# Optimization experiments

Hardware: AMD Instinct MI355X
Metric: run time of the kernel (lower is better)

The kernel has to match this reference:

```python
import jax, jax.numpy as jnp
import numpy as np

N_CLASSES = 19


def setup_inputs() -> dict:
    key = jax.random.key(0)
    k1, k2 = jax.random.split(key)
    embedding = jax.random.normal(k1, (4, 32, 128, 128), dtype=jnp.float32)
    label = jax.random.randint(k2, (4, 512, 512), 0, N_CLASSES, dtype=jnp.int64)
    return {"embedding": embedding, "label": label}


def _discriminative_loss(embedding, label, n_classes=N_CLASSES):
    N, H, W = label.shape
    C = embedding.shape[1]
    # bilinear upsample embedding to label resolution (F.upsample mode='bilinear')
    emb = jax.image.resize(embedding, (N, C, H, W), method="bilinear")
    HW = H * W
    emb = emb.reshape(N, C, HW).transpose(0, 2, 1)          # (N, HW, C)
    lab = label.reshape(N, HW)                               # (N, HW)

    onehot = jax.nn.one_hot(lab, n_classes, dtype=emb.dtype)  # (N, HW, K)
    count = onehot.sum(1)                                    # (N, K)
    mask = (count > 0).astype(emb.dtype)                     # (N, K)

    # per-class embedding sum and (biased, /(count+1)) mean
    cls_sum = jnp.einsum("npc,npk->nkc", emb, onehot)       # (N, K, C)
    cls_mean = cls_sum / (count[:, :, None] + 1.0)           # (N, K, C)

    # intra-class: per-pixel squared distance to own-class mean, mean over C
    mean_pp = jnp.take_along_axis(cls_mean, lab[:, :, None], axis=1)  # (N, HW, C)
    d2 = jnp.mean((emb - mean_pp) ** 2, axis=-1)             # (N, HW)
    intra_per_cls = jnp.einsum("np,npk->nk", d2, onehot) / (count + 1.0)  # (N, K)
    n_fg = mask[:, 1:].sum(1)                                # (N,)
    l2_intra = (intra_per_cls[:, 1:] * mask[:, 1:]).sum(1) / n_fg  # (N,)

    # inter-class: pairwise mean squared distance between class means
    diff = cls_mean[:, :, None, :] - cls_mean[:, None, :, :]  # (N, K, K, C)
    inter = jnp.mean(diff ** 2, axis=-1)                     # (N, K, K)
    inter = inter * mask[:, None, :] * mask[:, :, None]
    l2_inter = inter[:, 1:, 1:].reshape(N, -1).sum(1) / (n_fg * n_fg)  # (N,)

    return l2_intra - l2_inter


def reference(embedding, label):
    return _discriminative_loss(embedding, label)
```

## Files before the change

### kernel.cpp

```cpp
#include <hip/hip_runtime.h>

#define NIMG 4
#define NCLS 19
#define CCH  32
#define LH   128
#define LW   128
#define HH   512
#define WW   512
#define HWQ  (LH*LW)
#define HWP  (HH*WW)

#define TR 8
#define TC 8
#define NTX (LW/TC)
#define NTILE (256)
#define TCELLS (TR*TC)
#define RW 10
#define RING 100
#define NSLOT 608

__device__ __forceinline__ void taps(int v, int lim, int& i0, float& w0, float& w1) {
    int r = v & 3;
    int b = (v >> 2) + ((r < 2) ? -1 : 0);
    float f = 0.125f + 0.25f * (float)((r + 2) & 3);
    w0 = 1.f - f; w1 = f;
    if (b < 0)           { b = 0;       w0 = 1.f; w1 = 0.f; }
    else if (b >= lim)   { b = lim - 1; w0 = 0.f; w1 = 1.f; }
    i0 = b;
}

__device__ __forceinline__ float ring_fetch(const float* Gn, int i, int Y0, int X0) {
    int p = i / RING, r = i - p * RING;
    int gy = r / RW, gx = r - gy * RW;
    int yy = Y0 - 1 + gy; yy = yy < 0 ? 0 : (yy > LH - 1 ? LH - 1 : yy);
    int xx = X0 - 1 + gx; xx = xx < 0 ? 0 : (xx > LW - 1 ? LW - 1 : xx);
    return Gn[(size_t)p * HWQ + yy * LW + xx];
}

__global__ __launch_bounds__(256) void k_gram(const float* __restrict__ E,
        float* __restrict__ G) {
    int n = blockIdx.y, rp = blockIdx.x;
    int tid = threadIdx.x;
    int x = tid & 127, dy = tid >> 7;
    int y = rp * 2 + dy;
    int yn = (y < LH - 1) ? y + 1 : y;
    int xn = (x < LW - 1) ? x + 1 : x;
    bool fix = ((x & 63) == 63);
    const float* base = E + (size_t)n * CCH * HWQ;
    const float* Ea = base + y * LW + x;
    const float* Eb = base + yn * LW + x;
    const float* Eax = base + y * LW + xn;
    const float* Ebx = base + yn * LW + xn;
    float gs = 0.f, gh = 0.f, gv = 0.f, gda = 0.f;
#pragma unroll 8
    for (int c = 0; c < CCH; c++) {
        float a = Ea[(size_t)c * HWQ];
        float b = Eb[(size_t)c * HWQ];
        float ar = __shfl_down(a, 1);
        float br = __shfl_down(b, 1);
        if (fix) { ar = Eax[(size_t)c * HWQ]; br = Ebx[(size_t)c * HWQ]; }
        gs = fmaf(a, a, gs);
        gh = fmaf(a, ar, gh);
        gv = fmaf(a, b, gv);
        gda = fmaf(a, br, fmaf(ar, b, gda));
    }
    float* Gp = G + (size_t)n * 4 * HWQ + y * LW + x;
    Gp[0] = gs; Gp[HWQ] = gh; Gp[2 * HWQ] = gv; Gp[3 * HWQ] = gda;
}

__global__ __launch_bounds__(256, 4) void k_field(const float* __restrict__ E,
        const int* __restrict__ lab, const float* __restrict__ G,
        float* __restrict__ P_sum, float* __restrict__ P_cnt, float* __restrict__ P_S2) {
    int tile = blockIdx.x, n = blockIdx.y;
    int ty = tile >> 4, tx = tile & 15;
    int Y0 = ty * TR, X0 = tx * TC;
    __shared__ float A[TCELLS * NCLS];
    __shared__ float Gt[4 * RING];
    __shared__ float S2w[4 * NCLS];
    __shared__ float tmpc[NCLS * 8];
    __shared__ __align__(16) float cs_l[NSLOT];
    int tid = threadIdx.x;
    const int* ln = lab + (size_t)n * HWP;
    int h_lo = Y0 * 4 - 2;

    int hA, qA, hB = 0, qB = 0; bool vB;
    int4 LA, LB = make_int4(0, 0, 0, 0);
    {
        int hr = tid / RW, qi = tid - hr * RW;
        hA = h_lo + hr; qA = X0 - 1 + qi;
        int hc = hA < 0 ? 0 : (hA > HH - 1 ? HH - 1 : hA);
        int qc = qA < 0 ? 0 : (qA > LW - 1 ? LW - 1 : qA);
        LA = *(const int4*)(ln + hc * WW + (qc << 2));
    }
    vB = (tid < 360 - 256);
    if (vB) {
        int i = tid + 256;
        int hr = i / RW, qi = i - hr * RW;
        hB = h_lo + hr; qB = X0 - 1 + qi;
        int hc = hB < 0 ? 0 : (hB > HH - 1 ? HH - 1 : hB);
        int qc = qB < 0 ? 0 : (qB > LW - 1 ? LW - 1 : qB);
        LB = *(const int4*)(ln + hc * WW + (qc << 2));
    }
    int cc = tid >> 3, cy = tid & 7;
    const float* Er = E + ((size_t)n * CCH + cc) * HWQ + (Y0 + cy) * LW + X0;
    float4 ev0 = *(const float4*)Er;
    float4 ev1 = *(const float4*)(Er + 4);
    const float* Gn = G + (size_t)n * 4 * HWQ;
    float rv0 = ring_fetch(Gn, tid, Y0, X0);
    bool rB = (tid < 4 * RING - 256);
    float rv1 = rB ? ring_fetch(Gn, tid + 256, Y0, X0) : 0.f;

    for (int i = tid; i < TCELLS * NCLS; i += 256) A[i] = 0.f;
    if (tid < 4 * NCLS) S2w[tid] = 0.f;
    Gt[tid] = rv0;
    if (rB) Gt[tid + 256] = rv1;
    __syncthreads();

    const float* Gs_ = Gt, *Gh_ = Gt + RING, *Gv_ = Gt + 2 * RING, *Gda_ = Gt + 3 * RING;
    auto process = [&](int h, int q, int4 l4) {
        if (h < 0 || h >= HH || q < 0 || q >= LW) return;
        int y0; float wy0, wy1;
        taps(h, LH - 1, y0, wy0, wy1);
        int ry = y0 - Y0;
        bool r0 = (unsigned)ry < (unsigned)TR, r1 = (unsigned)(ry + 1) < (unsigned)TR;
        int rxm = q - 1 - X0, rx0 = q - X0, rxp = q + 1 - X0;
        bool bm = (unsigned)rxm < (unsigned)TC, b0 = (unsigned)rx0 < (unsigned)TC,
             bp = (unsigned)rxp < (unsigned)TC;
        bool fast = (q >= 1) && (q <= 126);
        bool owned = ((unsigned)(h - Y0 * 4) < 32u) && b0;
        if (fast) {
            if (r0) {
                int rb = (ry * TC) * NCLS;
                if (bm) { float* a = &A[rb + rxm * NCLS];
                    atomicAdd(a + l4.x, wy0 * 0.375f); atomicAdd(a + l4.y, wy0 * 0.125f); }
                if (b0) { float* a = &A[rb + rx0 * NCLS];
                    atomicAdd(a + l4.x, wy0 * 0.625f); atomicAdd(a + l4.y, wy0 * 0.875f);
                    atomicAdd(a + l4.z, wy0 * 0.875f); atomicAdd(a + l4.w, wy0 * 0.625f); }
                if (bp) { float* a = &A[rb + rxp * NCLS];
                    atomicAdd(a + l4.z, wy0 * 0.125f); atomicAdd(a + l4.w, wy0 * 0.375f); }
            }
            if (r1) {
                int rb = ((ry + 1) * TC) * NCLS;
                if (bm) { float* a = &A[rb + rxm * NCLS];
                    atomicAdd(a + l4.x, wy1 * 0.375f); atomicAdd(a + l4.y, wy1 * 0.125f); }
                if (b0) { float* a = &A[rb + rx0 * NCLS];
                    atomicAdd(a + l4.x, wy1 * 0.625f); atomicAdd(a + l4.y, wy1 * 0.875f);
                    atomicAdd(a + l4.z, wy1 * 0.875f); atomicAdd(a + l4.w, wy1 * 0.625f); }
                if (bp) { float* a = &A[rb + rxp * NCLS];
                    atomicAdd(a + l4.z, wy1 * 0.125f); atomicAdd(a + l4.w, wy1 * 0.375f); }
            }
            if (owned) {
                float u0 = wy0 * wy0, u1 = wy1 * wy1, u2t = 2.f * wy0 * wy1;
                int g00 = (y0 - Y0 + 1) * RW + rx0;
                float C0 = u0 * Gs_[g00]     + u1 * Gs_[g00 + RW]     + u2t * Gv_[g00];
                float C1 = u0 * Gs_[g00 + 1] + u1 * Gs_[g00 + RW + 1] + u2t * Gv_[g00 + 1];
                float C2 = u0 * Gs_[g00 + 2] + u1 * Gs_[g00 + RW + 2] + u2t * Gv_[g00 + 2];
                float D0 = 2.f * (u0 * Gh_[g00]     + u1 * Gh_[g00 + RW])     + u2t * Gda_[g00];
                float D1 = 2.f * (u0 * Gh_[g00 + 1] + u1 * Gh_[g00 + RW + 1]) + u2t * Gda_[g00 + 1];
                float d2a = fmaf(0.140625f, C0, fmaf(0.390625f, C1, 0.46875f * D0));
                float d2b = fmaf(0.015625f, C0, fmaf(0.765625f, C1, 0.21875f * D0));
                float d2c = fmaf(0.765625f, C1, fmaf(0.015625f, C2, 0.21875f * D1));
                float d2d = fmaf(0.390625f, C1, fmaf(0.140625f, C2, 0.46875f * D1));
                int wv = (tid >> 6) * NCLS;
                atomicAdd(&S2w[wv + l4.x], d2a); atomicAdd(&S2w[wv + l4.y], d2b);
                atomicAdd(&S2w[wv + l4.z], d2c); atomicAdd(&S2w[wv + l4.w], d2d);
            }
        } else {
            int Ls[4] = {l4.x, l4.y, l4.z, l4.w};
            float u0 = wy0 * wy0, u1 = wy1 * wy1, u2t = 2.f * wy0 * wy1;
            int gyr = y0 - Y0 + 1;
            int wv = (tid >> 6) * NCLS;
#pragma unroll
            for (int j = 0; j < 4; j++) {
                int w = (q << 2) + j;
                int x0; float wx0, wx1;
                taps(w, LW - 1, x0, wx0, wx1);
                int rxa = x0 - X0, rxb = rxa + 1;
                int L = Ls[j];
                if (r0) {
                    int rb = (ry * TC) * NCLS;
                    if ((unsigned)rxa < (unsigned)TC) atomicAdd(&A[rb + rxa * NCLS + L], wy0 * wx0);
                    if ((unsigned)rxb < (unsigned)TC) atomicAdd(&A[rb + rxb * NCLS + L], wy0 * wx1);
                }
                if (r1) {
                    int rb = ((ry + 1) * TC) * NCLS;
                    if ((unsigned)rxa < (unsigned)TC) atomicAdd(&A[rb + rxa * NCLS + L], wy1 * wx0);
                    if ((unsigned)rxb < (unsigned)TC) atomicAdd(&A[rb + rxb * NCLS + L], wy1 * wx1);
                }
                if (owned) {
                    int gg = gyr * RW + (x0 - X0 + 1);
                    float Ca = u0 * Gs_[gg]     + u1 * Gs_[gg + RW]     + u2t * Gv_[gg];
                    float Cb = u0 * Gs_[gg + 1] + u1 * Gs_[gg + RW + 1] + u2t * Gv_[gg + 1];
                    float Dd = 2.f * (u0 * Gh_[gg] + u1 * Gh_[gg + RW]) + u2t * Gda_[gg];
                    float d2 = wx0 * wx0 * Ca + wx1 * wx1 * Cb + 2.f * wx0 * wx1 * Dd;
                    atomicAdd(&S2w[wv + L], d2);
                }
            }
        }
    };
    process(hA, qA, LA);
    if (vB) process(hB, qB, LB);
    __syncthreads();

    {
        float ev[8] = {ev0.x, ev0.y, ev0.z, ev0.w, ev1.x, ev1.y, ev1.z, ev1.w};
        float acc[NCLS];
#pragma unroll
        for (int k = 0; k < NCLS; k++) acc[k] = 0.f;
#pragma unroll
        for (int cx = 0; cx < 8; cx++) {
            const float* Ar = &A[(cy * 8 + cx) * NCLS];
            float e = ev[cx];
#pragma unroll
            for (int k = 0; k < NCLS; k++) acc[k] = fmaf(Ar[k], e, acc[k]);
        }
#pragma unroll
        for (int k = 0; k < NCLS; k++) {
            acc[k] += __shfl_xor(acc[k], 1);
            acc[k] += __shfl_xor(acc[k], 2);
            acc[k] += __shfl_xor(acc[k], 4);
        }
        if (cy == 0) {
#pragma unroll
            for (int k = 0; k < NCLS; k++) cs_l[k * CCH + cc] = acc[k];
        }
    }
    if (tid < 8 * NCLS) {
        int g8 = tid / NCLS, k = tid - g8 * NCLS;
        float s = 0.f;
#pragma unroll
        for (int j = 0; j < 8; j++) s += A[(g8 * 8 + j) * NCLS + k];
        tmpc[k * 8 + g8] = s;
    }
    __syncthreads();

    float* Ps = P_sum + (size_t)(n * NTILE + tile) * NSLOT;
    if (tid < NSLOT / 4) ((float4*)Ps)[tid] = ((const float4*)cs_l)[tid];
    if (tid < NCLS) {
        float s = 0.f;
#pragma unroll
        for (int g8 = 0; g8 < 8; g8++) s += tmpc[tid * 8 + g8];
        P_cnt[(size_t)(n * NTILE + tile) * NCLS + tid] = s;
        P_S2[(size_t)(n * NTILE + tile) * NCLS + tid] =
            S2w[tid] + S2w[NCLS + tid] + S2w[2 * NCLS + tid] + S2w[3 * NCLS + tid];
    }
}

__global__ __launch_bounds__(256) void k_final(const float* __restrict__ P_sum,
        const float* __restrict__ P_cnt, const float* __restrict__ P_S2,
        float* __restrict__ out) {
    int n = blockIdx.x, tid = threadIdx.x;
    __shared__ double cs_d[NCLS * 33];
    __shared__ double m_d[NCLS * 33];
    __shared__ double cnt_d[NCLS], s2_d[NCLS];
    __shared__ double rk1[NCLS * 9], rk2[NCLS * 9];
    __shared__ double wpart[4];
    __shared__ double sIntra, sNfg;

    for (int i4 = tid; i4 < NSLOT / 4; i4 += 256) {
        const float4* p4 = (const float4*)(P_sum + (size_t)n * NTILE * NSLOT) + i4;
        double sx = 0.0, sy = 0.0, sz = 0.0, sw = 0.0;
#pragma unroll 4
        for (int t = 0; t < NTILE; t++) {
            float4 v = p4[(size_t)t * (NSLOT / 4)];
            sx += v.x; sy += v.y; sz += v.z; sw += v.w;
        }
        int idx = i4 * 4;
        int k = idx >> 5, c = idx & 31;
        cs_d[k * 33 + c] = sx; cs_d[k * 33 + c + 1] = sy;
        cs_d[k * 33 + c + 2] = sz; cs_d[k * 33 + c + 3] = sw;
    }
    if (tid < 8 * NCLS) {
        int k = tid >> 3, g = tid & 7;
        const float* p1 = P_cnt + ((size_t)n * NTILE + g * 32) * NCLS + k;
        const float* p2 = P_S2  + ((size_t)n * NTILE + g * 32) * NCLS + k;
        double s1 = 0.0, s2 = 0.0;
#pragma unroll 4
        for (int j = 0; j < 32; j++) { s1 += p1[j * NCLS]; s2 += p2[j * NCLS]; }
        rk1[k * 9 + g] = s1; rk2[k * 9 + g] = s2;
    }
    __syncthreads();
    if (tid < NCLS) {
        double s1 = 0.0, s2 = 0.0;
#pragma unroll
        for (int g = 0; g < 8; g++) { s1 += rk1[tid * 9 + g]; s2 += rk2[tid * 9 + g]; }
        cnt_d[tid] = s1; s2_d[tid] = s2;
    }
    __syncthreads();
    for (int idx = tid; idx < NSLOT; idx += 256) {
        int k = idx >> 5, c = idx & 31;
        m_d[k * 33 + c] = cs_d[k * 33 + c] / (cnt_d[k] + 1.0);
    }
    __syncthreads();
    double vi = 0.0, fg = 0.0;
    if (tid >= 1 && tid < NCLS && cnt_d[tid] > 0.0) {
        fg = 1.0;
        double dot = 0.0, mm = 0.0;
        for (int c = 0; c < CCH; c++) {
            double mv = m_d[tid * 33 + c];
            dot += mv * cs_d[tid * 33 + c];
            mm += mv * mv;
        }
        vi = (s2_d[tid] - 2.0 * dot + cnt_d[tid] * mm) * 0.03125 / (cnt_d[tid] + 1.0);
    }
    if (tid < 64) {
#pragma unroll
        for (int s_ = 32; s_ >= 1; s_ >>= 1) { vi += __shfl_xor(vi, s_); fg += __shfl_xor(fg, s_); }
        if (tid == 0) { sIntra = vi; sNfg = fg; }
    }
    double ve = 0.0;
    for (int t2 = tid; t2 < 324; t2 += 256) {
        int j = 1 + t2 / 18, k = 1 + t2 % 18;
        if (cnt_d[j] > 0.0 && cnt_d[k] > 0.0) {
            double s = 0.0;
            for (int c = 0; c < CCH; c++) {
                double d = m_d[j * 33 + c] - m_d[k * 33 + c];
                s += d * d;
            }
            ve += s * 0.03125;
        }
    }
#pragma unroll
    for (int s_ = 32; s_ >= 1; s_ >>= 1) ve += __shfl_xor(ve, s_);
    if ((tid & 63) == 0) wpart[tid >> 6] = ve;
    __syncthreads();
    if (tid == 0) {
        double inter = wpart[0] + wpart[1] + wpart[2] + wpart[3];
        out[n] = (float)(sIntra / sNfg - inter / (sNfg * sNfg));
    }
}

extern "C" void kernel_launch(void* const* d_in, const int* in_sizes, int n_in,
                              void* d_out, int out_size, void* d_ws, size_t ws_size,
                              hipStream_t stream) {
    const float* E = (const float*)d_in[0];
    const int* lab = (const int*)d_in[1];
    float* out = (float*)d_out;

    float* P_sum = (float*)d_ws;
    float* P_cnt = P_sum + (size_t)NIMG * NTILE * NSLOT;
    float* P_S2  = P_cnt + (size_t)NIMG * NTILE * NCLS;
    float* G     = P_S2  + (size_t)NIMG * NTILE * NCLS;

    k_gram <<<dim3(64, NIMG),    dim3(256), 0, stream>>>(E, G);
    k_field<<<dim3(NTILE, NIMG), dim3(256), 0, stream>>>(E, lab, G, P_sum, P_cnt, P_S2);
    k_final<<<dim3(NIMG),        dim3(256), 0, stream>>>(P_sum, P_cnt, P_S2, out);
}
```

Measured before the change: 141.4 us.

## Halve field tiles, transpose class accumulator layout, widen final reduction block

```diff
diff --git a/kernel.cpp b/kernel.cpp
--- a/kernel.cpp
+++ b/kernel.cpp
@@ -10,14 +10,17 @@
 #define HWQ  (LH*LW)
 #define HWP  (HH*WW)
 
-#define TR 8
+#define TR 4
 #define TC 8
-#define NTX (LW/TC)
-#define NTILE (256)
-#define TCELLS (TR*TC)
+#define NTX 16
+#define NTY 32
+#define NTILE 512
+#define TCELLS 32
 #define RW 10
-#define RING 100
+#define RROWS 6
+#define RING 60
 #define NSLOT 608
+#define HITEMS 200
 
 __device__ __forceinline__ void taps(int v, int lim, int& i0, float& w0, float& w1) {
     int r = v & 3;
@@ -68,57 +71,41 @@
     Gp[0] = gs; Gp[HWQ] = gh; Gp[2 * HWQ] = gv; Gp[3 * HWQ] = gda;
 }
 
-__global__ __launch_bounds__(256, 4) void k_field(const float* __restrict__ E,
+__global__ __launch_bounds__(256, 8) void k_field(const float* __restrict__ E,
         const int* __restrict__ lab, const float* __restrict__ G,
         float* __restrict__ P_sum, float* __restrict__ P_cnt, float* __restrict__ P_S2) {
     int tile = blockIdx.x, n = blockIdx.y;
     int ty = tile >> 4, tx = tile & 15;
     int Y0 = ty * TR, X0 = tx * TC;
-    __shared__ float A[TCELLS * NCLS];
+    __shared__ float A[NCLS * TCELLS];
     __shared__ float Gt[4 * RING];
-    __shared__ float S2w[4 * NCLS];
+    __shared__ float S2w[16 * NCLS];
     __shared__ float tmpc[NCLS * 8];
     __shared__ __align__(16) float cs_l[NSLOT];
     int tid = threadIdx.x;
+
     const int* ln = lab + (size_t)n * HWP;
     int h_lo = Y0 * 4 - 2;
-
-    int hA, qA, hB = 0, qB = 0; bool vB;
-    int4 LA, LB = make_int4(0, 0, 0, 0);
-    {
-        int hr = tid / RW, qi = tid - hr * RW;
-        hA = h_lo + hr; qA = X0 - 1 + qi;
-        int hc = hA < 0 ? 0 : (hA > HH - 1 ? HH - 1 : hA);
-        int qc = qA < 0 ? 0 : (qA > LW - 1 ? LW - 1 : qA);
-        LA = *(const int4*)(ln + hc * WW + (qc << 2));
-    }
-    vB = (tid < 360 - 256);
-    if (vB) {
-        int i = tid + 256;
-        int hr = i / RW, qi = i - hr * RW;
-        hB = h_lo + hr; qB = X0 - 1 + qi;
-        int hc = hB < 0 ? 0 : (hB > HH - 1 ? HH - 1 : hB);
-        int qc = qB < 0 ? 0 : (qB > LW - 1 ? LW - 1 : qB);
-        LB = *(const int4*)(ln + hc * WW + (qc << 2));
-    }
-    int cc = tid >> 3, cy = tid & 7;
-    const float* Er = E + ((size_t)n * CCH + cc) * HWQ + (Y0 + cy) * LW + X0;
-    float4 ev0 = *(const float4*)Er;
-    float4 ev1 = *(const float4*)(Er + 4);
+    int hr = tid / RW, qi = tid - hr * RW;
+    int h = h_lo + hr, q = X0 - 1 + qi;
+    int hc = h < 0 ? 0 : (h > HH - 1 ? HH - 1 : h);
+    int qc = q < 0 ? 0 : (q > LW - 1 ? LW - 1 : q);
+    int4 L4 = *(const int4*)(ln + hc * WW + (qc << 2));
+
+    int cc = tid >> 3, sub = tid & 7, cy = sub >> 1, hh = sub & 1;
+    const float* Er = E + ((size_t)n * CCH + cc) * HWQ + (Y0 + cy) * LW + X0 + hh * 4;
+    float4 ev = *(const float4*)Er;
+
     const float* Gn = G + (size_t)n * 4 * HWQ;
-    float rv0 = ring_fetch(Gn, tid, Y0, X0);
-    bool rB = (tid < 4 * RING - 256);
-    float rv1 = rB ? ring_fetch(Gn, tid + 256, Y0, X0) : 0.f;
-
-    for (int i = tid; i < TCELLS * NCLS; i += 256) A[i] = 0.f;
-    if (tid < 4 * NCLS) S2w[tid] = 0.f;
-    Gt[tid] = rv0;
-    if (rB) Gt[tid + 256] = rv1;
+    float rv = (tid < 4 * RING) ? ring_fetch(Gn, tid, Y0, X0) : 0.f;
+
+    for (int i = tid; i < NCLS * TCELLS; i += 256) A[i] = 0.f;
+    for (int i = tid; i < 16 * NCLS; i += 256) S2w[i] = 0.f;
+    if (tid < 4 * RING) Gt[tid] = rv;
     __syncthreads();
 
     const float* Gs_ = Gt, *Gh_ = Gt + RING, *Gv_ = Gt + 2 * RING, *Gda_ = Gt + 3 * RING;
-    auto process = [&](int h, int q, int4 l4) {
-        if (h < 0 || h >= HH || q < 0 || q >= LW) return;
+    if (tid < HITEMS && h >= 0 && h < HH && q >= 0 && q < LW) {
         int y0; float wy0, wy1;
         taps(h, LH - 1, y0, wy0, wy1);
         int ry = y0 - Y0;
@@ -127,27 +114,28 @@
         bool bm = (unsigned)rxm < (unsigned)TC, b0 = (unsigned)rx0 < (unsigned)TC,
              bp = (unsigned)rxp < (unsigned)TC;
         bool fast = (q >= 1) && (q <= 126);
-        bool owned = ((unsigned)(h - Y0 * 4) < 32u) && b0;
+        bool owned = ((unsigned)(h - Y0 * 4) < (unsigned)(TR * 4)) && b0;
+        int wv = (tid >> 4) * NCLS;
         if (fast) {
             if (r0) {
-                int rb = (ry * TC) * NCLS;
-                if (bm) { float* a = &A[rb + rxm * NCLS];
-                    atomicAdd(a + l4.x, wy0 * 0.375f); atomicAdd(a + l4.y, wy0 * 0.125f); }
-                if (b0) { float* a = &A[rb + rx0 * NCLS];
-                    atomicAdd(a + l4.x, wy0 * 0.625f); atomicAdd(a + l4.y, wy0 * 0.875f);
-                    atomicAdd(a + l4.z, wy0 * 0.875f); atomicAdd(a + l4.w, wy0 * 0.625f); }
-                if (bp) { float* a = &A[rb + rxp * NCLS];
-                    atomicAdd(a + l4.z, wy0 * 0.125f); atomicAdd(a + l4.w, wy0 * 0.375f); }
+                int rb = ry * TC;
+                if (bm) { float* a = &A[rb + rxm];
+                    atomicAdd(a + L4.x * TCELLS, wy0 * 0.375f); atomicAdd(a + L4.y * TCELLS, wy0 * 0.125f); }
+                if (b0) { float* a = &A[rb + rx0];
+                    atomicAdd(a + L4.x * TCELLS, wy0 * 0.625f); atomicAdd(a + L4.y * TCELLS, wy0 * 0.875f);
+                    atomicAdd(a + L4.z * TCELLS, wy0 * 0.875f); atomicAdd(a + L4.w * TCELLS, wy0 * 0.625f); }
+                if (bp) { float* a = &A[rb + rxp];
+                    atomicAdd(a + L4.z * TCELLS, wy0 * 0.125f); atomicAdd(a + L4.w * TCELLS, wy0 * 0.375f); }
             }
             if (r1) {
-                int rb = ((ry + 1) * TC) * NCLS;
-                if (bm) { float* a = &A[rb + rxm * NCLS];
-                    atomicAdd(a + l4.x, wy1 * 0.375f); atomicAdd(a + l4.y, wy1 * 0.125f); }
-                if (b0) { float* a = &A[rb + rx0 * NCLS];
-                    atomicAdd(a + l4.x, wy1 * 0.625f); atomicAdd(a + l4.y, wy1 * 0.875f);
-                    atomicAdd(a + l4.z, wy1 * 0.875f); atomicAdd(a + l4.w, wy1 * 0.625f); }
-                if (bp) { float* a = &A[rb + rxp * NCLS];
-                    atomicAdd(a + l4.z, wy1 * 0.125f); atomicAdd(a + l4.w, wy1 * 0.375f); }
+                int rb = (ry + 1) * TC;
+                if (bm) { float* a = &A[rb + rxm];
+                    atomicAdd(a + L4.x * TCELLS, wy1 * 0.375f); atomicAdd(a + L4.y * TCELLS, wy1 * 0.125f); }
+                if (b0) { float* a = &A[rb + rx0];
+                    atomicAdd(a + L4.x * TCELLS, wy1 * 0.625f); atomicAdd(a + L4.y * TCELLS, wy1 * 0.875f);
+                    atomicAdd(a + L4.z * TCELLS, wy1 * 0.875f); atomicAdd(a + L4.w * TCELLS, wy1 * 0.625f); }
+                if (bp) { float* a = &A[rb + rxp];
+                    atomicAdd(a + L4.z * TCELLS, wy1 * 0.125f); atomicAdd(a + L4.w * TCELLS, wy1 * 0.375f); }
             }
             if (owned) {
                 float u0 = wy0 * wy0, u1 = wy1 * wy1, u2t = 2.f * wy0 * wy1;
@@ -157,19 +145,17 @@
                 float C2 = u0 * Gs_[g00 + 2] + u1 * Gs_[g00 + RW + 2] + u2t * Gv_[g00 + 2];
                 float D0 = 2.f * (u0 * Gh_[g00]     + u1 * Gh_[g00 + RW])     + u2t * Gda_[g00];
                 float D1 = 2.f * (u0 * Gh_[g00 + 1] + u1 * Gh_[g00 + RW + 1]) + u2t * Gda_[g00 + 1];
-                float d2a = fmaf(0.140625f, C0, fmaf(0.390625f, C1, 0.46875f * D0));
-                float d2b = fmaf(0.015625f, C0, fmaf(0.765625f, C1, 0.21875f * D0));
-                float d2c = fmaf(0.765625f, C1, fmaf(0.015625f, C2, 0.21875f * D1));
-                float d2d = fmaf(0.390625f, C1, fmaf(0.140625f, C2, 0.46875f * D1));
-                int wv = (tid >> 6) * NCLS;
-                atomicAdd(&S2w[wv + l4.x], d2a); atomicAdd(&S2w[wv + l4.y], d2b);
-                atomicAdd(&S2w[wv + l4.z], d2c); atomicAdd(&S2w[wv + l4.w], d2d);
+                float d2a = fmaf(0.140625f, C0, fmaf(0.390625f, C1, 0.234375f * D0));
+                float d2b = fmaf(0.015625f, C0, fmaf(0.765625f, C1, 0.109375f * D0));
+                float d2c = fmaf(0.765625f, C1, fmaf(0.015625f, C2, 0.109375f * D1));
+                float d2d = fmaf(0.390625f, C1, fmaf(0.140625f, C2, 0.234375f * D1));
+                atomicAdd(&S2w[wv + L4.x], d2a); atomicAdd(&S2w[wv + L4.y], d2b);
+                atomicAdd(&S2w[wv + L4.z], d2c); atomicAdd(&S2w[wv + L4.w], d2d);
             }
         } else {
-            int Ls[4] = {l4.x, l4.y, l4.z, l4.w};
+            int Ls[4] = {L4.x, L4.y, L4.z, L4.w};
             float u0 = wy0 * wy0, u1 = wy1 * wy1, u2t = 2.f * wy0 * wy1;
             int gyr = y0 - Y0 + 1;
-            int wv = (tid >> 6) * NCLS;
 #pragma unroll
             for (int j = 0; j < 4; j++) {
                 int w = (q << 2) + j;
@@ -178,41 +164,40 @@
                 int rxa = x0 - X0, rxb = rxa + 1;
                 int L = Ls[j];
                 if (r0) {
-                    int rb = (ry * TC) * NCLS;
-                    if ((unsigned)rxa < (unsigned)TC) atomicAdd(&A[rb + rxa * NCLS + L], wy0 * wx0);
-                    if ((unsigned)rxb < (unsigned)TC) atomicAdd(&A[rb + rxb * NCLS + L], wy0 * wx1);
+                    int rb = ry * TC;
+                    if ((unsigned)rxa < (unsigned)TC) atomicAdd(&A[L * TCELLS + rb + rxa], wy0 * wx0);
+                    if ((unsigned)rxb < (unsigned)TC) atomicAdd(&A[L * TCELLS + rb + rxb], wy0 * wx1);
                 }
                 if (r1) {
-                    int rb = ((ry + 1) * TC) * NCLS;
-                    if ((unsigned)rxa < (unsigned)TC) atomicAdd(&A[rb + rxa * NCLS + L], wy1 * wx0);
-                    if ((unsigned)rxb < (unsigned)TC) atomicAdd(&A[rb + rxb * NCLS + L], wy1 * wx1);
+                    int rb = (ry + 1) * TC;
+                    if ((unsigned)rxa < (unsigned)TC) atomicAdd(&A[L * TCELLS + rb + rxa], wy1 * wx0);
+                    if ((unsigned)rxb < (unsigned)TC) atomicAdd(&A[L * TCELLS + rb + rxb], wy1 * wx1);
                 }
                 if (owned) {
                     int gg = gyr * RW + (x0 - X0 + 1);
                     float Ca = u0 * Gs_[gg]     + u1 * Gs_[gg + RW]     + u2t * Gv_[gg];
                     float Cb = u0 * Gs_[gg + 1] + u1 * Gs_[gg + RW + 1] + u2t * Gv_[gg + 1];
                     float Dd = 2.f * (u0 * Gh_[gg] + u1 * Gh_[gg + RW]) + u2t * Gda_[gg];
-                    float d2 = wx0 * wx0 * Ca + wx1 * wx1 * Cb + 2.f * wx0 * wx1 * Dd;
+                    float d2 = wx0 * wx0 * Ca + wx1 * wx1 * Cb + wx0 * wx1 * Dd;
                     atomicAdd(&S2w[wv + L], d2);
                 }
             }
         }
-    };
-    process(hA, qA, LA);
-    if (vB) process(hB, qB, LB);
+    }
     __syncthreads();
 
     {
-        float ev[8] = {ev0.x, ev0.y, ev0.z, ev0.w, ev1.x, ev1.y, ev1.z, ev1.w};
+        float ev_[4] = {ev.x, ev.y, ev.z, ev.w};
         float acc[NCLS];
 #pragma unroll
         for (int k = 0; k < NCLS; k++) acc[k] = 0.f;
-#pragma unroll
-        for (int cx = 0; cx < 8; cx++) {
-            const float* Ar = &A[(cy * 8 + cx) * NCLS];
-            float e = ev[cx];
-#pragma unroll
-            for (int k = 0; k < NCLS; k++) acc[k] = fmaf(Ar[k], e, acc[k]);
+        int base = cy * TC + hh * 4;
+#pragma unroll
+        for (int cx = 0; cx < 4; cx++) {
+            float e = ev_[cx];
+            const float* Ac = &A[base + cx];
+#pragma unroll
+            for (int k = 0; k < NCLS; k++) acc[k] = fmaf(Ac[k * TCELLS], e, acc[k]);
         }
 #pragma unroll
         for (int k = 0; k < NCLS; k++) {
@@ -220,7 +205,7 @@
             acc[k] += __shfl_xor(acc[k], 2);
             acc[k] += __shfl_xor(acc[k], 4);
         }
-        if (cy == 0) {
+        if (sub == 0) {
 #pragma unroll
             for (int k = 0; k < NCLS; k++) cs_l[k * CCH + cc] = acc[k];
         }
@@ -229,7 +214,7 @@
         int g8 = tid / NCLS, k = tid - g8 * NCLS;
         float s = 0.f;
 #pragma unroll
-        for (int j = 0; j < 8; j++) s += A[(g8 * 8 + j) * NCLS + k];
+        for (int j = 0; j < 4; j++) s += A[k * TCELLS + g8 * 4 + j];
         tmpc[k * 8 + g8] = s;
     }
     __syncthreads();
@@ -241,53 +226,76 @@
 #pragma unroll
         for (int g8 = 0; g8 < 8; g8++) s += tmpc[tid * 8 + g8];
         P_cnt[(size_t)(n * NTILE + tile) * NCLS + tid] = s;
-        P_S2[(size_t)(n * NTILE + tile) * NCLS + tid] =
-            S2w[tid] + S2w[NCLS + tid] + S2w[2 * NCLS + tid] + S2w[3 * NCLS + tid];
-    }
-}
-
-__global__ __launch_bounds__(256) void k_final(const float* __restrict__ P_sum,
+        float s2 = 0.f;
+#pragma unroll
+        for (int j = 0; j < 16; j++) s2 += S2w[j * NCLS + tid];
+        P_S2[(size_t)(n * NTILE + tile) * NCLS + tid] = s2;
+    }
+}
+
+__global__ __launch_bounds__(1024) void k_final(const float* __restrict__ P_sum,
         const float* __restrict__ P_cnt, const float* __restrict__ P_S2,
         float* __restrict__ out) {
     int n = blockIdx.x, tid = threadIdx.x;
+    __shared__ double wred[16 * NSLOT];
     __shared__ double cs_d[NCLS * 33];
     __shared__ double m_d[NCLS * 33];
     __shared__ double cnt_d[NCLS], s2_d[NCLS];
-    __shared__ double rk1[NCLS * 9], rk2[NCLS * 9];
-    __shared__ double wpart[4];
+    __shared__ double rkb1[64 * 20], rkb2[64 * 20];
+    __shared__ double wpart[16];
     __shared__ double sIntra, sNfg;
-
-    for (int i4 = tid; i4 < NSLOT / 4; i4 += 256) {
-        const float4* p4 = (const float4*)(P_sum + (size_t)n * NTILE * NSLOT) + i4;
-        double sx = 0.0, sy = 0.0, sz = 0.0, sw = 0.0;
-#pragma unroll 4
-        for (int t = 0; t < NTILE; t++) {
-            float4 v = p4[(size_t)t * (NSLOT / 4)];
-            sx += v.x; sy += v.y; sz += v.z; sw += v.w;
-        }
-        int idx = i4 * 4;
-        int k = idx >> 5, c = idx & 31;
-        cs_d[k * 33 + c] = sx; cs_d[k * 33 + c + 1] = sy;
-        cs_d[k * 33 + c + 2] = sz; cs_d[k * 33 + c + 3] = sw;
-    }
-    if (tid < 8 * NCLS) {
-        int k = tid >> 3, g = tid & 7;
-        const float* p1 = P_cnt + ((size_t)n * NTILE + g * 32) * NCLS + k;
-        const float* p2 = P_S2  + ((size_t)n * NTILE + g * 32) * NCLS + k;
+    int wv = tid >> 6, lane = tid & 63;
+
+    {
+        double a0x = 0, a0y = 0, a0z = 0, a0w = 0;
+        double a1x = 0, a1y = 0, a1z = 0, a1w = 0;
+        double a2x = 0, a2y = 0, a2z = 0, a2w = 0;
+        const float4* Pb = (const float4*)(P_sum + (size_t)n * NTILE * NSLOT);
+#pragma unroll 2
+        for (int t = wv; t < NTILE; t += 16) {
+            const float4* pt = Pb + (size_t)t * (NSLOT / 4);
+            float4 v0 = pt[lane];
+            float4 v1 = pt[lane + 64];
+            a0x += v0.x; a0y += v0.y; a0z += v0.z; a0w += v0.w;
+            a1x += v1.x; a1y += v1.y; a1z += v1.z; a1w += v1.w;
+            if (lane < 24) {
+                float4 v2 = pt[lane + 128];
+                a2x += v2.x; a2y += v2.y; a2z += v2.z; a2w += v2.w;
+            }
+        }
+        double* wr = wred + wv * NSLOT;
+        wr[lane * 4 + 0] = a0x; wr[lane * 4 + 1] = a0y;
+        wr[lane * 4 + 2] = a0z; wr[lane * 4 + 3] = a0w;
+        wr[(lane + 64) * 4 + 0] = a1x; wr[(lane + 64) * 4 + 1] = a1y;
+        wr[(lane + 64) * 4 + 2] = a1z; wr[(lane + 64) * 4 + 3] = a1w;
+        if (lane < 24) {
+            wr[(lane + 128) * 4 + 0] = a2x; wr[(lane + 128) * 4 + 1] = a2y;
+            wr[(lane + 128) * 4 + 2] = a2z; wr[(lane + 128) * 4 + 3] = a2w;
+        }
+    }
+    for (int idx = tid; idx < 64 * NCLS; idx += 1024) {
+        int g = idx / NCLS, k = idx - g * NCLS;
+        const float* p1 = P_cnt + ((size_t)n * NTILE + g * 8) * NCLS + k;
+        const float* p2 = P_S2  + ((size_t)n * NTILE + g * 8) * NCLS + k;
         double s1 = 0.0, s2 = 0.0;
-#pragma unroll 4
-        for (int j = 0; j < 32; j++) { s1 += p1[j * NCLS]; s2 += p2[j * NCLS]; }
-        rk1[k * 9 + g] = s1; rk2[k * 9 + g] = s2;
-    }
-    __syncthreads();
+#pragma unroll
+        for (int j = 0; j < 8; j++) { s1 += p1[j * NCLS]; s2 += p2[j * NCLS]; }
+        rkb1[g * 20 + k] = s1; rkb2[g * 20 + k] = s2;
+    }
+    __syncthreads();
+    for (int s = tid; s < NSLOT; s += 1024) {
+        double acc = 0.0;
+#pragma unroll
+        for (int w = 0; w < 16; w++) acc += wred[w * NSLOT + s];
+        cs_d[(s >> 5) * 33 + (s & 31)] = acc;
+    }
     if (tid < NCLS) {
         double s1 = 0.0, s2 = 0.0;
-#pragma unroll
-        for (int g = 0; g < 8; g++) { s1 += rk1[tid * 9 + g]; s2 += rk2[tid * 9 + g]; }
+        for (int g = 0; g < 64; g++) { s1 += rkb1[g * 20 + tid]; s2 += rkb2[g * 20 + tid]; }
         cnt_d[tid] = s1; s2_d[tid] = s2;
     }
     __syncthreads();
-    for (int idx = tid; idx < NSLOT; idx += 256) {
+    for (int idx = tid; idx < NSLOT; idx += 1024) {
         int k = idx >> 5, c = idx & 31;
         m_d[k * 33 + c] = cs_d[k * 33 + c] / (cnt_d[k] + 1.0);
     }
@@ -309,23 +317,25 @@
         if (tid == 0) { sIntra = vi; sNfg = fg; }
     }
     double ve = 0.0;
-    for (int t2 = tid; t2 < 324; t2 += 256) {
-        int j = 1 + t2 / 18, k = 1 + t2 % 18;
+    if (tid < 324) {
+        int j = 1 + tid / 18, k = 1 + tid % 18;
         if (cnt_d[j] > 0.0 && cnt_d[k] > 0.0) {
             double s = 0.0;
             for (int c = 0; c < CCH; c++) {
                 double d = m_d[j * 33 + c] - m_d[k * 33 + c];
                 s += d * d;
             }
-            ve += s * 0.03125;
+            ve = s * 0.03125;
         }
     }
 #pragma unroll
     for (int s_ = 32; s_ >= 1; s_ >>= 1) ve += __shfl_xor(ve, s_);
-    if ((tid & 63) == 0) wpart[tid >> 6] = ve;
+    if (lane == 0) wpart[wv] = ve;
     __syncthreads();
     if (tid == 0) {
-        double inter = wpart[0] + wpart[1] + wpart[2] + wpart[3];
+        double inter = 0.0;
+#pragma unroll
+        for (int w = 0; w < 16; w++) inter += wpart[w];
         out[n] = (float)(sIntra / sNfg - inter / (sNfg * sNfg));
     }
 }
@@ -342,7 +352,7 @@
     float* P_S2  = P_cnt + (size_t)NIMG * NTILE * NCLS;
     float* G     = P_S2  + (size_t)NIMG * NTILE * NCLS;
 
-    k_gram <<<dim3(64, NIMG),    dim3(256), 0, stream>>>(E, G);
-    k_field<<<dim3(NTILE, NIMG), dim3(256), 0, stream>>>(E, lab, G, P_sum, P_cnt, P_S2);
-    k_final<<<dim3(NIMG),        dim3(256), 0, stream>>>(P_sum, P_cnt, P_S2, out);
-}
+    k_gram <<<dim3(64, NIMG),    dim3(256),  0, stream>>>(E, G);
+    k_field<<<dim3(NTILE, NIMG), dim3(256),  0, stream>>>(E, lab, G, P_sum, P_cnt, P_S2);
+    k_final<<<dim3(NIMG),        dim3(1024), 0, stream>>>(P_sum, P_cnt, P_S2, out);
+}
```

Result: faster. 135.5 us (-4.2%).
